# Kernel tuning notes

Hardware: AMD Instinct MI355X
Metric: run time of the kernel (lower is better)

## Reference

```python
import jax, jax.numpy as jnp
import numpy as np

N_NODES = 50000
N_EDGES = 800000
H_NODE = 128
H_EDGE = 128
EPS = 1e-5


def _bn(x, gamma, beta):
    # training-mode BatchNorm1d over axis 0 (biased variance)
    mean = jnp.mean(x, axis=0)
    var = jnp.var(x, axis=0)
    return (x - mean) * jax.lax.rsqrt(var + EPS) * gamma + beta


def setup_inputs() -> dict:
    key = jax.random.key(0)
    ks = jax.random.split(key, 8)
    d_in = H_NODE + H_EDGE          # 256
    d_out = 2 * H_NODE              # 256
    bound = 1.0 / np.sqrt(d_in)
    return {
        "node_emb": jax.random.normal(ks[0], (N_NODES, H_NODE), jnp.float32),
        "edge_emb": jax.random.normal(ks[1], (N_EDGES, H_EDGE), jnp.float32),
        "i": jax.random.randint(ks[2], (N_EDGES,), 0, N_NODES, jnp.int64),
        "w1": jax.random.uniform(ks[3], (d_out, d_in), jnp.float32, -bound, bound),
        "b1": jax.random.uniform(ks[4], (d_out,), jnp.float32, -bound, bound),
        "g1": jnp.ones((d_out,), jnp.float32),
        "be1": jnp.zeros((d_out,), jnp.float32),
        "g2": jnp.ones((H_NODE,), jnp.float32),
        "be2": jnp.zeros((H_NODE,), jnp.float32),
    }


def reference(node_emb, edge_emb, i, w1, b1, g1, be1, g2, be2):
    # gather + concat: [E, H_NODE + H_EDGE]
    c1 = jnp.concatenate([node_emb[i], edge_emb], axis=1)
    # linear -> BN: [E, 2*H_NODE]
    c1 = _bn(c1 @ w1.T + b1, g1, be1)
    c1_filter, c1_core = jnp.split(c1, 2, axis=1)
    msg = jax.nn.sigmoid(c1_filter) * jnp.tanh(c1_core)  # [E, H_NODE]
    # scatter-sum back to nodes
    c1_emb = jax.ops.segment_sum(msg, i, num_segments=node_emb.shape[0])
    c1_emb = _bn(c1_emb, g2, be2)
    return jnp.tanh(node_emb + c1_emb)
```

## Files before the change

kernel.cpp:

```cpp
#include <hip/hip_runtime.h>
#include <hip/hip_fp16.h>
#include <cstdint>
#include <cstddef>

#define NN 50000
#define NE 800000
#define EPSV 1e-5f
#define NTILES (NE / 128)
#define PGRID 1024

typedef _Float16 f16_t;
typedef f16_t f16x8 __attribute__((ext_vector_type(8)));
typedef f16_t f16x4 __attribute__((ext_vector_type(4)));
typedef f16_t f16x2 __attribute__((ext_vector_type(2)));
typedef float f32x4 __attribute__((ext_vector_type(4)));

__device__ __forceinline__ float fast_tanh(float x) {
  float e2 = __expf(2.f * x);
  return 1.f - 2.f / (e2 + 1.f);
}
__device__ __forceinline__ float fast_sigmoid(float x) {
  return 1.f / (1.f + __expf(-x));
}

__launch_bounds__(256, 4)
__global__ void node_proj(const float* __restrict__ A, const float* __restrict__ w1,
                          const float* __restrict__ b1, f16_t* __restrict__ P) {
  __shared__ f16_t Alds[128][136];
  const int tid = threadIdx.x;
  const int wave = tid >> 6;
  const int lane = tid & 63;
  const int quad = lane >> 4;
  const int l16 = lane & 15;

  int cols[4];
#pragma unroll
  for (int nt = 0; nt < 4; ++nt) cols[nt] = 16 * wave + 64 * nt + l16;

  f16x8 bfrag[4][4];
#pragma unroll
  for (int nt = 0; nt < 4; ++nt)
#pragma unroll
    for (int ks = 0; ks < 4; ++ks) {
      const float* src = w1 + (size_t)cols[nt] * 256 + ks * 32 + quad * 8;
#pragma unroll
      for (int j = 0; j < 8; ++j) bfrag[nt][ks][j] = (f16_t)src[j];
    }

  float c0[4];
#pragma unroll
  for (int nt = 0; nt < 4; ++nt) c0[nt] = b1[cols[nt]];

  const int row0 = blockIdx.x * 128;
  {
    const int r = tid >> 1, half = tid & 1;
    const int grow = row0 + r;
    f16_t* dst = &Alds[r][half * 64];
    if (grow < NN) {
      const float4* src = (const float4*)(A + (size_t)grow * 128 + half * 64);
#pragma unroll
      for (int c = 0; c < 8; ++c) {
        float4 v0 = src[2 * c], v1 = src[2 * c + 1];
        f16x8 pk = {(f16_t)v0.x, (f16_t)v0.y, (f16_t)v0.z, (f16_t)v0.w,
                    (f16_t)v1.x, (f16_t)v1.y, (f16_t)v1.z, (f16_t)v1.w};
        *(f16x8*)(dst + c * 8) = pk;
      }
    } else {
      f16x8 z = {0, 0, 0, 0, 0, 0, 0, 0};
#pragma unroll
      for (int c = 0; c < 8; ++c) *(f16x8*)(dst + c * 8) = z;
    }
  }
  __syncthreads();

#pragma unroll 1
  for (int m = 0; m < 8; ++m) {
    f16x8 afrag[4];
#pragma unroll
    for (int ks = 0; ks < 4; ++ks)
      afrag[ks] = *(const f16x8*)&Alds[m * 16 + l16][ks * 32 + quad * 8];
    f32x4 acc[4];
#pragma unroll
    for (int nt = 0; nt < 4; ++nt) acc[nt] = (f32x4){0.f, 0.f, 0.f, 0.f};
#pragma unroll
    for (int ks = 0; ks < 4; ++ks)
#pragma unroll
      for (int nt = 0; nt < 4; ++nt)
        acc[nt] = __builtin_amdgcn_mfma_f32_16x16x32_f16(
            afrag[ks], bfrag[nt][ks], acc[nt], 0, 0, 0);
    const int rbase = row0 + m * 16 + quad * 4;
#pragma unroll
    for (int reg = 0; reg < 4; ++reg) {
      int g = rbase + reg;
      if (g < NN) {
        f16x4 pk;
#pragma unroll
        for (int nt = 0; nt < 4; ++nt) pk[nt] = (f16_t)(acc[nt][reg] + c0[nt]);
        *(f16x4*)&P[(size_t)g * 256 + wave * 64 + l16 * 4] = pk;
      }
    }
  }
}

template <int MODE>
__launch_bounds__(256, 4)
__global__ void edge_pass(const float* __restrict__ A, const float* __restrict__ w1,
                          const int* __restrict__ idx, const f16_t* __restrict__ P,
                          float* __restrict__ stats, const float* __restrict__ st,
                          f16_t* __restrict__ acc16, int* __restrict__ ctr) {
  __shared__ f16_t Alds[128][136];
  __shared__ int sIdx[128];
  __shared__ int s_tile;
  const int tid = threadIdx.x;
  const int wave = tid >> 6;
  const int lane = tid & 63;
  const int quad = lane >> 4;
  const int l16 = lane & 15;

  int cols[4];
#pragma unroll
  for (int nt = 0; nt < 4; ++nt) cols[nt] = 16 * wave + 64 * nt + l16;

  f16x8 bfrag[4][4];
#pragma unroll
  for (int nt = 0; nt < 4; ++nt)
#pragma unroll
    for (int ks = 0; ks < 4; ++ks) {
      const float* src = w1 + (size_t)cols[nt] * 256 + 128 + ks * 32 + quad * 8;
#pragma unroll
      for (int j = 0; j < 8; ++j) bfrag[nt][ks][j] = (f16_t)src[j];
    }

  float c0[4], c1c[4];
  if (MODE == 2) {
#pragma unroll
    for (int nt = 0; nt < 4; ++nt) {
      c0[nt] = st[cols[nt]];
      c1c[nt] = st[256 + cols[nt]];
    }
  }
  float ssum[4] = {0.f, 0.f, 0.f, 0.f};
  float ssq[4] = {0.f, 0.f, 0.f, 0.f};

  for (;;) {
    if (tid == 0) s_tile = atomicAdd(ctr, 1);
    __syncthreads();
    const int t = s_tile;
    if (t >= NTILES) break;
    const int row0 = t * 128;

    if (tid < 128) sIdx[tid] = idx[row0 + tid];
    {
      const int r = tid >> 1, half = tid & 1;
      const float4* src = (const float4*)(A + (size_t)(row0 + r) * 128 + half * 64);
      f16_t* dst = &Alds[r][half * 64];
#pragma unroll
      for (int c = 0; c < 8; ++c) {
        float4 v0 = src[2 * c], v1 = src[2 * c + 1];
        f16x8 pk = {(f16_t)v0.x, (f16_t)v0.y, (f16_t)v0.z, (f16_t)v0.w,
                    (f16_t)v1.x, (f16_t)v1.y, (f16_t)v1.z, (f16_t)v1.w};
        *(f16x8*)(dst + c * 8) = pk;
      }
    }
    __syncthreads();

#pragma unroll 1
    for (int m = 0; m < 8; ++m) {
      f16x8 afrag[4];
#pragma unroll
      for (int ks = 0; ks < 4; ++ks)
        afrag[ks] = *(const f16x8*)&Alds[m * 16 + l16][ks * 32 + quad * 8];

      int node[4];
      f16x4 pv[4];
#pragma unroll
      for (int reg = 0; reg < 4; ++reg) {
        node[reg] = sIdx[m * 16 + quad * 4 + reg];
        pv[reg] = *(const f16x4*)&P[(size_t)node[reg] * 256 + wave * 64 + l16 * 4];
      }

      f32x4 acc[4];
#pragma unroll
      for (int nt = 0; nt < 4; ++nt) acc[nt] = (f32x4){0.f, 0.f, 0.f, 0.f};
#pragma unroll
      for (int ks = 0; ks < 4; ++ks)
#pragma unroll
        for (int nt = 0; nt < 4; ++nt)
          acc[nt] = __builtin_amdgcn_mfma_f32_16x16x32_f16(
              afrag[ks], bfrag[nt][ks], acc[nt], 0, 0, 0);

#pragma unroll
      for (int reg = 0; reg < 4; ++reg) {
        float h[4];
#pragma unroll
        for (int nt = 0; nt < 4; ++nt) h[nt] = acc[nt][reg] + (float)pv[reg][nt];
        if (MODE == 1) {
#pragma unroll
          for (int nt = 0; nt < 4; ++nt) {
            ssum[nt] += h[nt];
            ssq[nt] += h[nt] * h[nt];
          }
        } else {
          float hn[4];
#pragma unroll
          for (int nt = 0; nt < 4; ++nt) hn[nt] = h[nt] * c0[nt] + c1c[nt];
          float msg0 = fast_sigmoid(hn[0]) * fast_tanh(hn[2]);
          float msg1 = fast_sigmoid(hn[1]) * fast_tanh(hn[3]);
          float o0 = __shfl_xor(msg0, 1);
          float o1 = __shfl_xor(msg1, 1);
          const bool ev = (l16 & 1) == 0;
          f16x2 val;
          val[0] = (f16_t)(ev ? msg0 : o1);
          val[1] = (f16_t)(ev ? o0 : msg1);
          const int colb = 16 * wave + (ev ? 0 : 64) + (l16 & ~1);
          __half2* addr = (__half2*)&acc16[(size_t)node[reg] * 128 + colb];
          unsafeAtomicAdd(addr, *(__half2*)&val);
        }
      }
    }
    __syncthreads();
  }

  if (MODE == 1) {
#pragma unroll
    for (int nt = 0; nt < 4; ++nt) {
      float s = ssum[nt], q = ssq[nt];
      s += __shfl_xor(s, 16); s += __shfl_xor(s, 32);
      q += __shfl_xor(q, 16); q += __shfl_xor(q, 32);
      if (quad == 0) {
        atomicAdd(&stats[cols[nt]], s);
        atomicAdd(&stats[256 + cols[nt]], q);
      }
    }
  }
}

__global__ void finalize1(const float* __restrict__ stats, const float* __restrict__ g1,
                          const float* __restrict__ be1, float* __restrict__ st) {
  int j = threadIdx.x;
  float mean = stats[j] * (1.f / NE);
  float var = stats[256 + j] * (1.f / NE) - mean * mean;
  float s = g1[j] * rsqrtf(var + EPSV);
  st[j] = s;
  st[256 + j] = be1[j] - mean * s;
}

__global__ void bn2_stats(const f16_t* __restrict__ acc16, float* __restrict__ stats) {
  const int tid = threadIdx.x;
  const int c2 = tid & 63;
  const int ph = tid >> 6;
  float s0 = 0.f, s1 = 0.f, q0 = 0.f, q1 = 0.f;
  for (int row = blockIdx.x * 4 + ph; row < NN; row += gridDim.x * 4) {
    f16x2 v = *(const f16x2*)&acc16[(size_t)row * 128 + 2 * c2];
    float a = (float)v[0], b = (float)v[1];
    s0 += a; q0 += a * a;
    s1 += b; q1 += b * b;
  }
  __shared__ float red[256][4];
  red[tid][0] = s0; red[tid][1] = s1; red[tid][2] = q0; red[tid][3] = q1;
  __syncthreads();
  if (ph == 0) {
    float a0 = 0.f, a1 = 0.f, b0 = 0.f, b1 = 0.f;
#pragma unroll
    for (int p = 0; p < 4; ++p) {
      a0 += red[p * 64 + c2][0]; a1 += red[p * 64 + c2][1];
      b0 += red[p * 64 + c2][2]; b1 += red[p * 64 + c2][3];
    }
    atomicAdd(&stats[2 * c2], a0);
    atomicAdd(&stats[2 * c2 + 1], a1);
    atomicAdd(&stats[128 + 2 * c2], b0);
    atomicAdd(&stats[128 + 2 * c2 + 1], b1);
  }
}

__global__ void finalize2(const float* __restrict__ stats, const float* __restrict__ g2,
                          const float* __restrict__ be2, float* __restrict__ sc) {
  int j = threadIdx.x;
  float mean = stats[j] * (1.f / NN);
  float var = stats[128 + j] * (1.f / NN) - mean * mean;
  float s = g2[j] * rsqrtf(var + EPSV);
  sc[j] = s;
  sc[128 + j] = be2[j] - mean * s;
}

__global__ void final_kernel(const float* __restrict__ node_emb, const float* __restrict__ sc,
                             const f16_t* __restrict__ acc16, float* __restrict__ out) {
  int i = blockIdx.x * blockDim.x + threadIdx.x;
  if (i >= NN * 32) return;
  int c4 = i & 31;
  int row = i >> 5;
  float4 s4 = ((const float4*)sc)[c4];
  float4 h4 = ((const float4*)(sc + 128))[c4];
  float4 ne = ((const float4*)node_emb)[i];
  f16x4 cv = *(const f16x4*)&acc16[(size_t)row * 128 + c4 * 4];
  float4 r;
  r.x = fast_tanh(ne.x + (float)cv[0] * s4.x + h4.x);
  r.y = fast_tanh(ne.y + (float)cv[1] * s4.y + h4.y);
  r.z = fast_tanh(ne.z + (float)cv[2] * s4.z + h4.z);
  r.w = fast_tanh(ne.w + (float)cv[3] * s4.w + h4.w);
  ((float4*)out)[i] = r;
}

extern "C" void kernel_launch(void* const* d_in, const int* in_sizes, int n_in,
                              void* d_out, int out_size, void* d_ws, size_t ws_size,
                              hipStream_t stream) {
  (void)in_sizes; (void)n_in; (void)ws_size; (void)out_size;
  const float* node_emb = (const float*)d_in[0];
  const float* edge_emb = (const float*)d_in[1];
  const int* idx = (const int*)d_in[2];
  const float* w1 = (const float*)d_in[3];
  const float* b1 = (const float*)d_in[4];
  const float* g1 = (const float*)d_in[5];
  const float* be1 = (const float*)d_in[6];
  const float* g2 = (const float*)d_in[7];
  const float* be2 = (const float*)d_in[8];
  float* out = (float*)d_out;

  float* wsf = (float*)d_ws;
  float* bn1sums = wsf;
  float* st = wsf + 512;
  float* bn2sums = wsf + 1024;
  float* sc2 = wsf + 1280;
  int* ctr1 = (int*)(wsf + 1536);
  int* ctr2 = (int*)(wsf + 1537);
  f16_t* P = (f16_t*)((char*)d_ws + 8192);
  f16_t* acc16 = (f16_t*)((char*)d_ws + 8192 + (size_t)NN * 256 * 2);

  hipMemsetAsync(wsf, 0, 2048 * sizeof(float), stream);
  hipMemsetAsync(acc16, 0, (size_t)NN * 128 * 2, stream);

  node_proj<<<(NN + 127) / 128, 256, 0, stream>>>(node_emb, w1, b1, P);
  edge_pass<1><<<PGRID, 256, 0, stream>>>(edge_emb, w1, idx, P, bn1sums, nullptr,
                                          nullptr, ctr1);
  finalize1<<<1, 256, 0, stream>>>(bn1sums, g1, be1, st);
  edge_pass<2><<<PGRID, 256, 0, stream>>>(edge_emb, w1, idx, P, nullptr, st,
                                          acc16, ctr2);
  bn2_stats<<<128, 256, 0, stream>>>(acc16, bn2sums);
  finalize2<<<1, 128, 0, stream>>>(bn2sums, g2, be2, sc2);
  final_kernel<<<(NN * 32 + 255) / 256, 256, 0, stream>>>(node_emb, sc2, acc16, out);
}
```

Before: 1.048 ms.

## Materialize pre-BN edge activations in fp16 instead of recomputing the second edge pass

The stats pass now also writes the pre-BatchNorm linear outputs for every edge to a workspace buffer in fp16, in a swizzled layout. A new elementwise kernel reads that buffer back, applies the BN affine, the gating and the scatter atomics. This replaces the second full pass that reread edge_emb and recomputed the MFMA GEMM. It trades a roughly 400MB re-read plus recompute for about 400MB written and 400MB read back, needs a much larger workspace, and falls back to the old path if the workspace is too small.

```diff
diff --git a/kernel.cpp b/kernel.cpp
--- a/kernel.cpp
+++ b/kernel.cpp
@@ -194,13 +194,7 @@
         float h[4];
 #pragma unroll
         for (int nt = 0; nt < 4; ++nt) h[nt] = acc[nt][reg] + (float)pv[reg][nt];
-        if (MODE == 1) {
-#pragma unroll
-          for (int nt = 0; nt < 4; ++nt) {
-            ssum[nt] += h[nt];
-            ssq[nt] += h[nt] * h[nt];
-          }
-        } else {
+        if (MODE == 2) {
           float hn[4];
 #pragma unroll
           for (int nt = 0; nt < 4; ++nt) hn[nt] = h[nt] * c0[nt] + c1c[nt];
@@ -215,13 +209,26 @@
           const int colb = 16 * wave + (ev ? 0 : 64) + (l16 & ~1);
           __half2* addr = (__half2*)&acc16[(size_t)node[reg] * 128 + colb];
           unsafeAtomicAdd(addr, *(__half2*)&val);
+        } else {
+#pragma unroll
+          for (int nt = 0; nt < 4; ++nt) {
+            ssum[nt] += h[nt];
+            ssq[nt] += h[nt] * h[nt];
+          }
+          if (MODE == 3) {
+            f16x4 hp;
+#pragma unroll
+            for (int nt = 0; nt < 4; ++nt) hp[nt] = (f16_t)h[nt];
+            const int edge = row0 + m * 16 + quad * 4 + reg;
+            *(f16x4*)&acc16[(size_t)edge * 256 + wave * 64 + l16 * 4] = hp;
+          }
         }
       }
     }
     __syncthreads();
   }
 
-  if (MODE == 1) {
+  if (MODE == 1 || MODE == 3) {
 #pragma unroll
     for (int nt = 0; nt < 4; ++nt) {
       float s = ssum[nt], q = ssq[nt];
@@ -236,13 +243,49 @@
 }
 
 __global__ void finalize1(const float* __restrict__ stats, const float* __restrict__ g1,
-                          const float* __restrict__ be1, float* __restrict__ st) {
+                          const float* __restrict__ be1, float* __restrict__ st,
+                          float* __restrict__ st_sw) {
   int j = threadIdx.x;
   float mean = stats[j] * (1.f / NE);
   float var = stats[256 + j] * (1.f / NE) - mean * mean;
   float s = g1[j] * rsqrtf(var + EPSV);
+  float t = be1[j] - mean * s;
   st[j] = s;
-  st[256 + j] = be1[j] - mean * s;
+  st[256 + j] = t;
+  int w = (j & 63) >> 4, nt = j >> 6, l16 = j & 15;
+  int p = w * 64 + l16 * 4 + nt;
+  st_sw[p] = s;
+  st_sw[256 + p] = t;
+}
+
+__launch_bounds__(256, 8)
+__global__ void edge_apply(const f16_t* __restrict__ hsw, const int* __restrict__ idx,
+                           const float* __restrict__ stw, f16_t* __restrict__ acc16) {
+  const int i = blockIdx.x * 256 + threadIdx.x;
+  const int e = i >> 5;
+  const int k2 = i & 31;
+  const int node = idx[e];
+  const f16x8 h8 = *(const f16x8*)&hsw[(size_t)e * 256 + k2 * 8];
+  const float4* sv = (const float4*)stw;
+  const float4 s0 = sv[2 * k2], s1 = sv[2 * k2 + 1];
+  const float4 t0 = sv[64 + 2 * k2], t1 = sv[64 + 2 * k2 + 1];
+  const float hn0 = (float)h8[0] * s0.x + t0.x;
+  const float hn1 = (float)h8[1] * s0.y + t0.y;
+  const float hn2 = (float)h8[2] * s0.z + t0.z;
+  const float hn3 = (float)h8[3] * s0.w + t0.w;
+  const float hn4 = (float)h8[4] * s1.x + t1.x;
+  const float hn5 = (float)h8[5] * s1.y + t1.y;
+  const float hn6 = (float)h8[6] * s1.z + t1.z;
+  const float hn7 = (float)h8[7] * s1.w + t1.w;
+  f16x2 va, vb;
+  va[0] = (f16_t)(fast_sigmoid(hn0) * fast_tanh(hn2));
+  va[1] = (f16_t)(fast_sigmoid(hn4) * fast_tanh(hn6));
+  vb[0] = (f16_t)(fast_sigmoid(hn1) * fast_tanh(hn3));
+  vb[1] = (f16_t)(fast_sigmoid(hn5) * fast_tanh(hn7));
+  f16_t* rowp = acc16 + (size_t)node * 128;
+  const int cA = 16 * (k2 >> 3) + ((k2 & 7) << 1);
+  unsafeAtomicAdd((__half2*)(rowp + cA), *(__half2*)&va);
+  unsafeAtomicAdd((__half2*)(rowp + 64 + cA), *(__half2*)&vb);
 }
 
 __global__ void bn2_stats(const f16_t* __restrict__ acc16, float* __restrict__ stats) {
@@ -304,7 +347,7 @@
 extern "C" void kernel_launch(void* const* d_in, const int* in_sizes, int n_in,
                               void* d_out, int out_size, void* d_ws, size_t ws_size,
                               hipStream_t stream) {
-  (void)in_sizes; (void)n_in; (void)ws_size; (void)out_size;
+  (void)in_sizes; (void)n_in; (void)out_size;
   const float* node_emb = (const float*)d_in[0];
   const float* edge_emb = (const float*)d_in[1];
   const int* idx = (const int*)d_in[2];
@@ -323,18 +366,29 @@
   float* sc2 = wsf + 1280;
   int* ctr1 = (int*)(wsf + 1536);
   int* ctr2 = (int*)(wsf + 1537);
-  f16_t* P = (f16_t*)((char*)d_ws + 8192);
-  f16_t* acc16 = (f16_t*)((char*)d_ws + 8192 + (size_t)NN * 256 * 2);
+  float* st_sw = wsf + 2048;
+  char* base = (char*)d_ws + 16384;
+  f16_t* P = (f16_t*)base;
+  f16_t* acc16 = (f16_t*)(base + (size_t)NN * 512);
+  f16_t* hsw = (f16_t*)(base + (size_t)NN * 512 + (size_t)NN * 256);
+  const size_t need = 16384 + (size_t)NN * 512 + (size_t)NN * 256 + (size_t)NE * 512;
 
   hipMemsetAsync(wsf, 0, 2048 * sizeof(float), stream);
-  hipMemsetAsync(acc16, 0, (size_t)NN * 128 * 2, stream);
+  hipMemsetAsync(acc16, 0, (size_t)NN * 256, stream);
 
   node_proj<<<(NN + 127) / 128, 256, 0, stream>>>(node_emb, w1, b1, P);
-  edge_pass<1><<<PGRID, 256, 0, stream>>>(edge_emb, w1, idx, P, bn1sums, nullptr,
-                                          nullptr, ctr1);
-  finalize1<<<1, 256, 0, stream>>>(bn1sums, g1, be1, st);
-  edge_pass<2><<<PGRID, 256, 0, stream>>>(edge_emb, w1, idx, P, nullptr, st,
-                                          acc16, ctr2);
+  if (ws_size >= need) {
+    edge_pass<3><<<PGRID, 256, 0, stream>>>(edge_emb, w1, idx, P, bn1sums, nullptr,
+                                            hsw, ctr1);
+    finalize1<<<1, 256, 0, stream>>>(bn1sums, g1, be1, st, st_sw);
+    edge_apply<<<NE * 32 / 256, 256, 0, stream>>>(hsw, idx, st_sw, acc16);
+  } else {
+    edge_pass<1><<<PGRID, 256, 0, stream>>>(edge_emb, w1, idx, P, bn1sums, nullptr,
+                                            nullptr, ctr1);
+    finalize1<<<1, 256, 0, stream>>>(bn1sums, g1, be1, st, st_sw);
+    edge_pass<2><<<PGRID, 256, 0, stream>>>(edge_emb, w1, idx, P, nullptr, st,
+                                            acc16, ctr2);
+  }
   bn2_stats<<<128, 256, 0, stream>>>(acc16, bn2sums);
   finalize2<<<1, 128, 0, stream>>>(bn2sums, g2, be2, sc2);
   final_kernel<<<(NN * 32 + 255) / 256, 256, 0, stream>>>(node_emb, sc2, acc16, out);
```

After: 901.8 us. 1.16x faster.

## Store pre-BN edge activations once and apply BN/gating in a separate pass

Applied to the files above, without the earlier changes.

Removes the second full edge pass that recomputed the GEMM and re-read the fp32 edge embeddings. The first pass now writes pre-BN activations as fp16 to a workspace buffer in a swizzled layout, and a lightweight elementwise kernel applies BN1, the gate and the scatter-add. The fused pass also uses 512-thread blocks with 32-row tiles and double-buffered async global-to-LDS copies with an XOR swizzle. The trade is writing and then re-reading a 400MB fp16 intermediate in exchange for skipping the recompute and the second fp32 read.

```diff
diff --git a/kernel.cpp b/kernel.cpp
--- a/kernel.cpp
+++ b/kernel.cpp
@@ -6,8 +6,8 @@
 #define NN 50000
 #define NE 800000
 #define EPSV 1e-5f
-#define NTILES (NE / 128)
-#define PGRID 1024
+#define NT32 (NE / 32)
+#define PGRID2 512
 
 typedef _Float16 f16_t;
 typedef f16_t f16x8 __attribute__((ext_vector_type(8)));
@@ -21,6 +21,17 @@
 }
 __device__ __forceinline__ float fast_sigmoid(float x) {
   return 1.f / (1.f + __expf(-x));
+}
+
+__device__ __forceinline__ void async_cp16(const void* g, void* l) {
+  __builtin_amdgcn_global_load_lds(
+      (const __attribute__((address_space(1))) unsigned int*)g,
+      (__attribute__((address_space(3))) unsigned int*)l, 16, 0, 0);
+}
+__device__ __forceinline__ void async_cp4(const void* g, void* l) {
+  __builtin_amdgcn_global_load_lds(
+      (const __attribute__((address_space(1))) unsigned int*)g,
+      (__attribute__((address_space(3))) unsigned int*)l, 4, 0, 0);
 }
 
 __launch_bounds__(256, 4)
@@ -93,156 +104,173 @@
     for (int reg = 0; reg < 4; ++reg) {
       int g = rbase + reg;
       if (g < NN) {
-        f16x4 pk;
-#pragma unroll
-        for (int nt = 0; nt < 4; ++nt) pk[nt] = (f16_t)(acc[nt][reg] + c0[nt]);
-        *(f16x4*)&P[(size_t)g * 256 + wave * 64 + l16 * 4] = pk;
-      }
-    }
-  }
-}
-
-template <int MODE>
-__launch_bounds__(256, 4)
-__global__ void edge_pass(const float* __restrict__ A, const float* __restrict__ w1,
-                          const int* __restrict__ idx, const f16_t* __restrict__ P,
-                          float* __restrict__ stats, const float* __restrict__ st,
-                          f16_t* __restrict__ acc16, int* __restrict__ ctr) {
-  __shared__ f16_t Alds[128][136];
-  __shared__ int sIdx[128];
-  __shared__ int s_tile;
+        f16x2 pA, pB;
+        pA[0] = (f16_t)(acc[0][reg] + c0[0]);
+        pA[1] = (f16_t)(acc[2][reg] + c0[2]);
+        pB[0] = (f16_t)(acc[1][reg] + c0[1]);
+        pB[1] = (f16_t)(acc[3][reg] + c0[3]);
+        *(f16x2*)&P[(size_t)g * 256 + wave * 32 + l16 * 2] = pA;
+        *(f16x2*)&P[(size_t)g * 256 + (wave + 4) * 32 + l16 * 2] = pB;
+      }
+    }
+  }
+}
+
+__launch_bounds__(512, 4)
+__global__ void edge_fused(const float* __restrict__ A, const float* __restrict__ w1,
+                           const int* __restrict__ idx, const f16_t* __restrict__ P,
+                           float* __restrict__ stats, f16_t* __restrict__ Hs,
+                           int* __restrict__ ctr) {
+  __shared__ float AldsF[2][4096];
+  __shared__ int sIdx[2][32];
+  __shared__ int s_nx[2];
   const int tid = threadIdx.x;
-  const int wave = tid >> 6;
+  const int w = tid >> 6;
   const int lane = tid & 63;
   const int quad = lane >> 4;
   const int l16 = lane & 15;
 
-  int cols[4];
-#pragma unroll
-  for (int nt = 0; nt < 4; ++nt) cols[nt] = 16 * wave + 64 * nt + l16;
-
-  f16x8 bfrag[4][4];
-#pragma unroll
-  for (int nt = 0; nt < 4; ++nt)
+  int cols[2];
+#pragma unroll
+  for (int n = 0; n < 2; ++n) cols[n] = 16 * w + 128 * n + l16;
+
+  f16x8 bfrag[2][4];
+#pragma unroll
+  for (int n = 0; n < 2; ++n)
 #pragma unroll
     for (int ks = 0; ks < 4; ++ks) {
-      const float* src = w1 + (size_t)cols[nt] * 256 + 128 + ks * 32 + quad * 8;
-#pragma unroll
-      for (int j = 0; j < 8; ++j) bfrag[nt][ks][j] = (f16_t)src[j];
-    }
-
-  float c0[4], c1c[4];
-  if (MODE == 2) {
-#pragma unroll
-    for (int nt = 0; nt < 4; ++nt) {
-      c0[nt] = st[cols[nt]];
-      c1c[nt] = st[256 + cols[nt]];
-    }
-  }
-  float ssum[4] = {0.f, 0.f, 0.f, 0.f};
-  float ssq[4] = {0.f, 0.f, 0.f, 0.f};
-
-  for (;;) {
-    if (tid == 0) s_tile = atomicAdd(ctr, 1);
+      const float* src = w1 + (size_t)cols[n] * 256 + 128 + ks * 32 + quad * 8;
+#pragma unroll
+      for (int j = 0; j < 8; ++j) bfrag[n][ks][j] = (f16_t)src[j];
+    }
+
+  const int r0 = 4 * w + (lane >> 5);
+  const int r1 = r0 + 2;
+  const int cswz = (lane & 31) * 16;
+  const int so0 = r0 * 512 + (cswz ^ ((r0 & 7) << 4));
+  const int so1 = r1 * 512 + (cswz ^ ((r1 & 7) << 4));
+  const int xoffF = (quad * 8) ^ ((l16 & 7) << 2);
+
+  float ssum[2] = {0.f, 0.f};
+  float ssq[2] = {0.f, 0.f};
+
+  if (tid == 0) s_nx[0] = atomicAdd(ctr, 1);
+  __syncthreads();
+  int t = s_nx[0];
+  int p = 0;
+  if (t < NT32) {
+    const char* gb = (const char*)A + (size_t)t * 16384;
+    async_cp16(gb + so0, (char*)&AldsF[0][0] + (2 * w + 0) * 1024);
+    async_cp16(gb + so1, (char*)&AldsF[0][0] + (2 * w + 1) * 1024);
+    if (w == 0 && lane < 32) async_cp4(idx + t * 32 + lane, &sIdx[0][0]);
+  }
+
+  while (t < NT32) {
+    if (tid == 0) s_nx[p ^ 1] = atomicAdd(ctr, 1);
+    asm volatile("s_waitcnt vmcnt(0)" ::: "memory");
     __syncthreads();
-    const int t = s_tile;
-    if (t >= NTILES) break;
-    const int row0 = t * 128;
-
-    if (tid < 128) sIdx[tid] = idx[row0 + tid];
-    {
-      const int r = tid >> 1, half = tid & 1;
-      const float4* src = (const float4*)(A + (size_t)(row0 + r) * 128 + half * 64);
-      f16_t* dst = &Alds[r][half * 64];
-#pragma unroll
-      for (int c = 0; c < 8; ++c) {
-        float4 v0 = src[2 * c], v1 = src[2 * c + 1];
-        f16x8 pk = {(f16_t)v0.x, (f16_t)v0.y, (f16_t)v0.z, (f16_t)v0.w,
-                    (f16_t)v1.x, (f16_t)v1.y, (f16_t)v1.z, (f16_t)v1.w};
-        *(f16x8*)(dst + c * 8) = pk;
-      }
-    }
-    __syncthreads();
-
-#pragma unroll 1
-    for (int m = 0; m < 8; ++m) {
-      f16x8 afrag[4];
-#pragma unroll
-      for (int ks = 0; ks < 4; ++ks)
-        afrag[ks] = *(const f16x8*)&Alds[m * 16 + l16][ks * 32 + quad * 8];
-
+    const int tn = s_nx[p ^ 1];
+    if (tn < NT32) {
+      const char* gb = (const char*)A + (size_t)tn * 16384;
+      async_cp16(gb + so0, (char*)&AldsF[p ^ 1][0] + (2 * w + 0) * 1024);
+      async_cp16(gb + so1, (char*)&AldsF[p ^ 1][0] + (2 * w + 1) * 1024);
+      if (w == 0 && lane < 32) async_cp4(idx + tn * 32 + lane, &sIdx[p ^ 1][0]);
+    }
+
+    const float* buf = &AldsF[p][0];
+#pragma unroll
+    for (int m = 0; m < 2; ++m) {
       int node[4];
-      f16x4 pv[4];
+      f16x2 pvv[4];
 #pragma unroll
       for (int reg = 0; reg < 4; ++reg) {
-        node[reg] = sIdx[m * 16 + quad * 4 + reg];
-        pv[reg] = *(const f16x4*)&P[(size_t)node[reg] * 256 + wave * 64 + l16 * 4];
-      }
-
-      f32x4 acc[4];
-#pragma unroll
-      for (int nt = 0; nt < 4; ++nt) acc[nt] = (f32x4){0.f, 0.f, 0.f, 0.f};
-#pragma unroll
-      for (int ks = 0; ks < 4; ++ks)
-#pragma unroll
-        for (int nt = 0; nt < 4; ++nt)
-          acc[nt] = __builtin_amdgcn_mfma_f32_16x16x32_f16(
-              afrag[ks], bfrag[nt][ks], acc[nt], 0, 0, 0);
-
+        node[reg] = sIdx[p][m * 16 + quad * 4 + reg];
+        pvv[reg] = *(const f16x2*)&P[(size_t)node[reg] * 256 + w * 32 + l16 * 2];
+      }
+      f16x8 afr[4];
+      const int rb = (m * 16 + l16) * 128;
+#pragma unroll
+      for (int ks = 0; ks < 4; ++ks) {
+        const int fa = rb + ks * 32 + xoffF;
+        float4 u = *(const float4*)&buf[fa];
+        float4 v = *(const float4*)&buf[fa ^ 4];
+        afr[ks] = (f16x8){(f16_t)u.x, (f16_t)u.y, (f16_t)u.z, (f16_t)u.w,
+                          (f16_t)v.x, (f16_t)v.y, (f16_t)v.z, (f16_t)v.w};
+      }
+      f32x4 acc[2];
+      acc[0] = (f32x4){0.f, 0.f, 0.f, 0.f};
+      acc[1] = (f32x4){0.f, 0.f, 0.f, 0.f};
+#pragma unroll
+      for (int ks = 0; ks < 4; ++ks) {
+        acc[0] = __builtin_amdgcn_mfma_f32_16x16x32_f16(afr[ks], bfrag[0][ks],
+                                                        acc[0], 0, 0, 0);
+        acc[1] = __builtin_amdgcn_mfma_f32_16x16x32_f16(afr[ks], bfrag[1][ks],
+                                                        acc[1], 0, 0, 0);
+      }
+      const int ebase = t * 32 + m * 16 + quad * 4;
 #pragma unroll
       for (int reg = 0; reg < 4; ++reg) {
-        float h[4];
-#pragma unroll
-        for (int nt = 0; nt < 4; ++nt) h[nt] = acc[nt][reg] + (float)pv[reg][nt];
-        if (MODE == 1) {
-#pragma unroll
-          for (int nt = 0; nt < 4; ++nt) {
-            ssum[nt] += h[nt];
-            ssq[nt] += h[nt] * h[nt];
-          }
-        } else {
-          float hn[4];
-#pragma unroll
-          for (int nt = 0; nt < 4; ++nt) hn[nt] = h[nt] * c0[nt] + c1c[nt];
-          float msg0 = fast_sigmoid(hn[0]) * fast_tanh(hn[2]);
-          float msg1 = fast_sigmoid(hn[1]) * fast_tanh(hn[3]);
-          float o0 = __shfl_xor(msg0, 1);
-          float o1 = __shfl_xor(msg1, 1);
-          const bool ev = (l16 & 1) == 0;
-          f16x2 val;
-          val[0] = (f16_t)(ev ? msg0 : o1);
-          val[1] = (f16_t)(ev ? o0 : msg1);
-          const int colb = 16 * wave + (ev ? 0 : 64) + (l16 & ~1);
-          __half2* addr = (__half2*)&acc16[(size_t)node[reg] * 128 + colb];
-          unsafeAtomicAdd(addr, *(__half2*)&val);
-        }
-      }
-    }
-    __syncthreads();
-  }
-
-  if (MODE == 1) {
-#pragma unroll
-    for (int nt = 0; nt < 4; ++nt) {
-      float s = ssum[nt], q = ssq[nt];
-      s += __shfl_xor(s, 16); s += __shfl_xor(s, 32);
-      q += __shfl_xor(q, 16); q += __shfl_xor(q, 32);
-      if (quad == 0) {
-        atomicAdd(&stats[cols[nt]], s);
-        atomicAdd(&stats[256 + cols[nt]], q);
-      }
+        float h0 = acc[0][reg] + (float)pvv[reg][0];
+        float h1 = acc[1][reg] + (float)pvv[reg][1];
+        ssum[0] += h0; ssq[0] += h0 * h0;
+        ssum[1] += h1; ssq[1] += h1 * h1;
+        f16x2 hp = {(f16_t)h0, (f16_t)h1};
+        *(f16x2*)&Hs[(size_t)(ebase + reg) * 256 + w * 32 + l16 * 2] = hp;
+      }
+    }
+    t = tn;
+    p ^= 1;
+  }
+
+#pragma unroll
+  for (int n = 0; n < 2; ++n) {
+    float s = ssum[n], q = ssq[n];
+    s += __shfl_xor(s, 16); s += __shfl_xor(s, 32);
+    q += __shfl_xor(q, 16); q += __shfl_xor(q, 32);
+    if (quad == 0) {
+      atomicAdd(&stats[cols[n]], s);
+      atomicAdd(&stats[256 + cols[n]], q);
     }
   }
 }
 
 __global__ void finalize1(const float* __restrict__ stats, const float* __restrict__ g1,
-                          const float* __restrict__ be1, float* __restrict__ st) {
+                          const float* __restrict__ be1, float* __restrict__ st_sw) {
   int j = threadIdx.x;
   float mean = stats[j] * (1.f / NE);
   float var = stats[256 + j] * (1.f / NE) - mean * mean;
   float s = g1[j] * rsqrtf(var + EPSV);
-  st[j] = s;
-  st[256 + j] = be1[j] - mean * s;
+  float t = be1[j] - mean * s;
+  int pos = ((j >> 4) & 7) * 32 + (j & 15) * 2 + (j >> 7);
+  st_sw[pos] = s;
+  st_sw[256 + pos] = t;
+}
+
+__launch_bounds__(256, 8)
+__global__ void edge_apply(const f16_t* __restrict__ hsw, const int* __restrict__ idx,
+                           const float* __restrict__ stw, f16_t* __restrict__ acc16) {
+  const int i = blockIdx.x * 256 + threadIdx.x;
+  const int e = i >> 5;
+  const int k2 = i & 31;
+  const int node = idx[e];
+  const f16x8 h8 = *(const f16x8*)&hsw[(size_t)e * 256 + k2 * 8];
+  const float4 sA = *(const float4*)&stw[8 * k2];
+  const float4 sB = *(const float4*)&stw[8 * k2 + 4];
+  const float4 tA = *(const float4*)&stw[256 + 8 * k2];
+  const float4 tB = *(const float4*)&stw[256 + 8 * k2 + 4];
+  f16x2 va, vb;
+  va[0] = (f16_t)(fast_sigmoid((float)h8[0] * sA.x + tA.x) *
+                  fast_tanh((float)h8[1] * sA.y + tA.y));
+  va[1] = (f16_t)(fast_sigmoid((float)h8[2] * sA.z + tA.z) *
+                  fast_tanh((float)h8[3] * sA.w + tA.w));
+  vb[0] = (f16_t)(fast_sigmoid((float)h8[4] * sB.x + tB.x) *
+                  fast_tanh((float)h8[5] * sB.y + tB.y));
+  vb[1] = (f16_t)(fast_sigmoid((float)h8[6] * sB.z + tB.z) *
+                  fast_tanh((float)h8[7] * sB.w + tB.w));
+  const int c = 16 * (k2 >> 2) + 4 * (k2 & 3);
+  f16_t* rowp = acc16 + (size_t)node * 128;
+  unsafeAtomicAdd((__half2*)(rowp + c), *(__half2*)&va);
+  unsafeAtomicAdd((__half2*)(rowp + c + 2), *(__half2*)&vb);
 }
 
 __global__ void bn2_stats(const f16_t* __restrict__ acc16, float* __restrict__ stats) {
@@ -304,7 +332,7 @@
 extern "C" void kernel_launch(void* const* d_in, const int* in_sizes, int n_in,
                               void* d_out, int out_size, void* d_ws, size_t ws_size,
                               hipStream_t stream) {
-  (void)in_sizes; (void)n_in; (void)ws_size; (void)out_size;
+  (void)in_sizes; (void)n_in; (void)out_size; (void)ws_size;
   const float* node_emb = (const float*)d_in[0];
   const float* edge_emb = (const float*)d_in[1];
   const int* idx = (const int*)d_in[2];
@@ -318,23 +346,22 @@
 
   float* wsf = (float*)d_ws;
   float* bn1sums = wsf;
-  float* st = wsf + 512;
+  float* st_sw = wsf + 512;
   float* bn2sums = wsf + 1024;
   float* sc2 = wsf + 1280;
   int* ctr1 = (int*)(wsf + 1536);
-  int* ctr2 = (int*)(wsf + 1537);
-  f16_t* P = (f16_t*)((char*)d_ws + 8192);
-  f16_t* acc16 = (f16_t*)((char*)d_ws + 8192 + (size_t)NN * 256 * 2);
+  char* base = (char*)d_ws + 8192;
+  f16_t* P = (f16_t*)base;
+  f16_t* acc16 = (f16_t*)(base + (size_t)NN * 512);
+  f16_t* hsw = (f16_t*)(base + (size_t)NN * 512 + (size_t)NN * 256);
 
   hipMemsetAsync(wsf, 0, 2048 * sizeof(float), stream);
-  hipMemsetAsync(acc16, 0, (size_t)NN * 128 * 2, stream);
+  hipMemsetAsync(acc16, 0, (size_t)NN * 256, stream);
 
   node_proj<<<(NN + 127) / 128, 256, 0, stream>>>(node_emb, w1, b1, P);
-  edge_pass<1><<<PGRID, 256, 0, stream>>>(edge_emb, w1, idx, P, bn1sums, nullptr,
-                                          nullptr, ctr1);
-  finalize1<<<1, 256, 0, stream>>>(bn1sums, g1, be1, st);
-  edge_pass<2><<<PGRID, 256, 0, stream>>>(edge_emb, w1, idx, P, nullptr, st,
-                                          acc16, ctr2);
+  edge_fused<<<PGRID2, 512, 0, stream>>>(edge_emb, w1, idx, P, bn1sums, hsw, ctr1);
+  finalize1<<<1, 256, 0, stream>>>(bn1sums, g1, be1, st_sw);
+  edge_apply<<<NE * 32 / 256, 256, 0, stream>>>(hsw, idx, st_sw, acc16);
   bn2_stats<<<128, 256, 0, stream>>>(acc16, bn2sums);
   finalize2<<<1, 128, 0, stream>>>(bn2sums, g2, be2, sc2);
   final_kernel<<<(NN * 32 + 255) / 256, 256, 0, stream>>>(node_emb, sc2, acc16, out);
```

New measurement: 1.163 ms. 1.11x slower.

## Fold BN finalize kernels into consumers and prefetch next P gather

Applied to the files above, without the earlier changes.

Removes the two single-block finalize kernels: edge_pass MODE 2 and final_kernel now compute the BN scale and shift directly from the accumulated sums, which saves two launches and their serialization. Inside the edge loop, the P gather for the next 16-row group is issued before the MFMAs of the current group, so the global gather latency overlaps with matrix math. MFMA sections are also wrapped in s_setprio. The cost is redundant per-thread rsqrt work and more live registers, which could lower occupancy. On the last group the prefetch wraps around and reloads group 0, which is harmless but wasted.

```diff
diff --git a/kernel.cpp b/kernel.cpp
--- a/kernel.cpp
+++ b/kernel.cpp
@@ -106,8 +106,9 @@
 __launch_bounds__(256, 4)
 __global__ void edge_pass(const float* __restrict__ A, const float* __restrict__ w1,
                           const int* __restrict__ idx, const f16_t* __restrict__ P,
-                          float* __restrict__ stats, const float* __restrict__ st,
-                          f16_t* __restrict__ acc16, int* __restrict__ ctr) {
+                          float* __restrict__ stats, const float* __restrict__ g1,
+                          const float* __restrict__ be1, f16_t* __restrict__ acc16,
+                          int* __restrict__ ctr) {
   __shared__ f16_t Alds[128][136];
   __shared__ int sIdx[128];
   __shared__ int s_tile;
@@ -135,8 +136,12 @@
   if (MODE == 2) {
 #pragma unroll
     for (int nt = 0; nt < 4; ++nt) {
-      c0[nt] = st[cols[nt]];
-      c1c[nt] = st[256 + cols[nt]];
+      const int c = cols[nt];
+      float mean = stats[c] * (1.f / NE);
+      float var = stats[256 + c] * (1.f / NE) - mean * mean;
+      float s = g1[c] * rsqrtf(var + EPSV);
+      c0[nt] = s;
+      c1c[nt] = be1[c] - mean * s;
     }
   }
   float ssum[4] = {0.f, 0.f, 0.f, 0.f};
@@ -164,43 +169,48 @@
     }
     __syncthreads();
 
+    int nodeC[4];
+    f16x4 pvC[4];
+#pragma unroll
+    for (int reg = 0; reg < 4; ++reg) {
+      nodeC[reg] = sIdx[quad * 4 + reg];
+      pvC[reg] = *(const f16x4*)&P[(size_t)nodeC[reg] * 256 + wave * 64 + l16 * 4];
+    }
+
 #pragma unroll 1
     for (int m = 0; m < 8; ++m) {
+      const int mm = (m + 1) & 7;
+      int nodeN[4];
+      f16x4 pvN[4];
+#pragma unroll
+      for (int reg = 0; reg < 4; ++reg) {
+        nodeN[reg] = sIdx[mm * 16 + quad * 4 + reg];
+        pvN[reg] = *(const f16x4*)&P[(size_t)nodeN[reg] * 256 + wave * 64 + l16 * 4];
+      }
+
       f16x8 afrag[4];
 #pragma unroll
       for (int ks = 0; ks < 4; ++ks)
         afrag[ks] = *(const f16x8*)&Alds[m * 16 + l16][ks * 32 + quad * 8];
 
-      int node[4];
-      f16x4 pv[4];
-#pragma unroll
-      for (int reg = 0; reg < 4; ++reg) {
-        node[reg] = sIdx[m * 16 + quad * 4 + reg];
-        pv[reg] = *(const f16x4*)&P[(size_t)node[reg] * 256 + wave * 64 + l16 * 4];
-      }
-
       f32x4 acc[4];
 #pragma unroll
       for (int nt = 0; nt < 4; ++nt) acc[nt] = (f32x4){0.f, 0.f, 0.f, 0.f};
+      __builtin_amdgcn_s_setprio(1);
 #pragma unroll
       for (int ks = 0; ks < 4; ++ks)
 #pragma unroll
         for (int nt = 0; nt < 4; ++nt)
           acc[nt] = __builtin_amdgcn_mfma_f32_16x16x32_f16(
               afrag[ks], bfrag[nt][ks], acc[nt], 0, 0, 0);
+      __builtin_amdgcn_s_setprio(0);
 
 #pragma unroll
       for (int reg = 0; reg < 4; ++reg) {
         float h[4];
 #pragma unroll
-        for (int nt = 0; nt < 4; ++nt) h[nt] = acc[nt][reg] + (float)pv[reg][nt];
-        if (MODE == 1) {
-#pragma unroll
-          for (int nt = 0; nt < 4; ++nt) {
-            ssum[nt] += h[nt];
-            ssq[nt] += h[nt] * h[nt];
-          }
-        } else {
+        for (int nt = 0; nt < 4; ++nt) h[nt] = acc[nt][reg] + (float)pvC[reg][nt];
+        if (MODE == 2) {
           float hn[4];
 #pragma unroll
           for (int nt = 0; nt < 4; ++nt) hn[nt] = h[nt] * c0[nt] + c1c[nt];
@@ -213,9 +223,20 @@
           val[0] = (f16_t)(ev ? msg0 : o1);
           val[1] = (f16_t)(ev ? o0 : msg1);
           const int colb = 16 * wave + (ev ? 0 : 64) + (l16 & ~1);
-          __half2* addr = (__half2*)&acc16[(size_t)node[reg] * 128 + colb];
+          __half2* addr = (__half2*)&acc16[(size_t)nodeC[reg] * 128 + colb];
           unsafeAtomicAdd(addr, *(__half2*)&val);
+        } else {
+#pragma unroll
+          for (int nt = 0; nt < 4; ++nt) {
+            ssum[nt] += h[nt];
+            ssq[nt] += h[nt] * h[nt];
+          }
         }
+      }
+#pragma unroll
+      for (int reg = 0; reg < 4; ++reg) {
+        nodeC[reg] = nodeN[reg];
+        pvC[reg] = pvN[reg];
       }
     }
     __syncthreads();
@@ -233,16 +254,6 @@
       }
     }
   }
-}
-
-__global__ void finalize1(const float* __restrict__ stats, const float* __restrict__ g1,
-                          const float* __restrict__ be1, float* __restrict__ st) {
-  int j = threadIdx.x;
-  float mean = stats[j] * (1.f / NE);
-  float var = stats[256 + j] * (1.f / NE) - mean * mean;
-  float s = g1[j] * rsqrtf(var + EPSV);
-  st[j] = s;
-  st[256 + j] = be1[j] - mean * s;
 }
 
 __global__ void bn2_stats(const f16_t* __restrict__ acc16, float* __restrict__ stats) {
@@ -273,24 +284,30 @@
   }
 }
 
-__global__ void finalize2(const float* __restrict__ stats, const float* __restrict__ g2,
-                          const float* __restrict__ be2, float* __restrict__ sc) {
-  int j = threadIdx.x;
-  float mean = stats[j] * (1.f / NN);
-  float var = stats[128 + j] * (1.f / NN) - mean * mean;
-  float s = g2[j] * rsqrtf(var + EPSV);
-  sc[j] = s;
-  sc[128 + j] = be2[j] - mean * s;
-}
-
-__global__ void final_kernel(const float* __restrict__ node_emb, const float* __restrict__ sc,
+__global__ void final_kernel(const float* __restrict__ node_emb,
+                             const float* __restrict__ bn2sums,
+                             const float* __restrict__ g2, const float* __restrict__ be2,
                              const f16_t* __restrict__ acc16, float* __restrict__ out) {
   int i = blockIdx.x * blockDim.x + threadIdx.x;
   if (i >= NN * 32) return;
   int c4 = i & 31;
   int row = i >> 5;
-  float4 s4 = ((const float4*)sc)[c4];
-  float4 h4 = ((const float4*)(sc + 128))[c4];
+  float4 sm = ((const float4*)bn2sums)[c4];
+  float4 sq = ((const float4*)(bn2sums + 128))[c4];
+  float4 g = ((const float4*)g2)[c4];
+  float4 b = ((const float4*)be2)[c4];
+  float4 s4, h4;
+  {
+    float mean, var;
+    mean = sm.x * (1.f / NN); var = sq.x * (1.f / NN) - mean * mean;
+    s4.x = g.x * rsqrtf(var + EPSV); h4.x = b.x - mean * s4.x;
+    mean = sm.y * (1.f / NN); var = sq.y * (1.f / NN) - mean * mean;
+    s4.y = g.y * rsqrtf(var + EPSV); h4.y = b.y - mean * s4.y;
+    mean = sm.z * (1.f / NN); var = sq.z * (1.f / NN) - mean * mean;
+    s4.z = g.z * rsqrtf(var + EPSV); h4.z = b.z - mean * s4.z;
+    mean = sm.w * (1.f / NN); var = sq.w * (1.f / NN) - mean * mean;
+    s4.w = g.w * rsqrtf(var + EPSV); h4.w = b.w - mean * s4.w;
+  }
   float4 ne = ((const float4*)node_emb)[i];
   f16x4 cv = *(const f16x4*)&acc16[(size_t)row * 128 + c4 * 4];
   float4 r;
@@ -304,7 +321,7 @@
 extern "C" void kernel_launch(void* const* d_in, const int* in_sizes, int n_in,
                               void* d_out, int out_size, void* d_ws, size_t ws_size,
                               hipStream_t stream) {
-  (void)in_sizes; (void)n_in; (void)ws_size; (void)out_size;
+  (void)in_sizes; (void)n_in; (void)out_size; (void)ws_size;
   const float* node_emb = (const float*)d_in[0];
   const float* edge_emb = (const float*)d_in[1];
   const int* idx = (const int*)d_in[2];
@@ -318,24 +335,22 @@
 
   float* wsf = (float*)d_ws;
   float* bn1sums = wsf;
-  float* st = wsf + 512;
-  float* bn2sums = wsf + 1024;
-  float* sc2 = wsf + 1280;
-  int* ctr1 = (int*)(wsf + 1536);
-  int* ctr2 = (int*)(wsf + 1537);
-  f16_t* P = (f16_t*)((char*)d_ws + 8192);
-  f16_t* acc16 = (f16_t*)((char*)d_ws + 8192 + (size_t)NN * 256 * 2);
-
-  hipMemsetAsync(wsf, 0, 2048 * sizeof(float), stream);
-  hipMemsetAsync(acc16, 0, (size_t)NN * 128 * 2, stream);
+  float* bn2sums = wsf + 512;
+  int* ctr1 = (int*)(wsf + 768);
+  int* ctr2 = (int*)(wsf + 769);
+  char* base = (char*)d_ws + 8192;
+  f16_t* P = (f16_t*)base;
+  f16_t* acc16 = (f16_t*)(base + (size_t)NN * 512);
+
+  hipMemsetAsync(wsf, 0, 1024 * sizeof(float), stream);
+  hipMemsetAsync(acc16, 0, (size_t)NN * 256, stream);
 
   node_proj<<<(NN + 127) / 128, 256, 0, stream>>>(node_emb, w1, b1, P);
-  edge_pass<1><<<PGRID, 256, 0, stream>>>(edge_emb, w1, idx, P, bn1sums, nullptr,
+  edge_pass<1><<<PGRID, 256, 0, stream>>>(edge_emb, w1, idx, P, bn1sums, g1, be1,
                                           nullptr, ctr1);
-  finalize1<<<1, 256, 0, stream>>>(bn1sums, g1, be1, st);
-  edge_pass<2><<<PGRID, 256, 0, stream>>>(edge_emb, w1, idx, P, nullptr, st,
+  edge_pass<2><<<PGRID, 256, 0, stream>>>(edge_emb, w1, idx, P, bn1sums, g1, be1,
                                           acc16, ctr2);
   bn2_stats<<<128, 256, 0, stream>>>(acc16, bn2sums);
-  finalize2<<<1, 128, 0, stream>>>(bn2sums, g2, be2, sc2);
-  final_kernel<<<(NN * 32 + 255) / 256, 256, 0, stream>>>(node_emb, sc2, acc16, out);
-}
+  final_kernel<<<(NN * 32 + 255) / 256, 256, 0, stream>>>(node_emb, bn2sums, g2,
+                                                          be2, acc16, out);
+}
```

New measurement: 1.092 ms. +4.1%, slower.
